# Optimization experiments

Measured on AMD Instinct MI355X. Metric: run time of the kernel, lower is better.

## Reference

```python
import jax, jax.numpy as jnp
import numpy as np

IMG = 4320
FM = 1080            # reduced image size after two stride-2 maxpools
F = 21               # RPN feature map size ((1080-50)//50 + 1)
NUM_ANCHORS = 6
SCALE = (IMG / 4.0) / (IMG / 200.0)   # input_shape/cnn_output_shape = 50.0
CONF = 0.95
K = 5                # bounding_box_limit


def _anchor_boxes():
    sizes = [1.0, 2.0]; ars = [0.5, 1.0, 2.0]
    base = np.array([[0.0, s * -(ar - 1) / 2, s, s * (1 + (ar - 1) / 2)]
                     for s in sizes for ar in ars], np.float32)        # (6,4)
    g = np.arange(F, dtype=np.float32)
    xg = np.broadcast_to(g[:, None], (F, F))
    yg = np.broadcast_to(g[None, :], (F, F))
    pos = np.stack([xg, yg, xg, yg], 0)                                # (4,F,F)
    return jnp.asarray(base[:, :, None, None] + pos[None])             # (6,4,F,F)


def _conv(x, w, b, stride, pad):
    y = jax.lax.conv_general_dilated(x, w, (stride, stride), [(pad, pad), (pad, pad)],
                                     dimension_numbers=('NCHW', 'OIHW', 'NCHW'))
    return y + b[None, :, None, None]


def _maxpool2(x):
    return jax.lax.reduce_window(x, -jnp.inf, jax.lax.max, (1, 1, 2, 2), (1, 1, 2, 2), 'VALID')


def _apply_offsets(a, o):
    # faithful to apply_bounding_box_offsets_to_anchors (note callers swap args)
    return jnp.stack([a[:, 0] + o[:, 0] - o[:, 2] / 2,
                      a[:, 1] - o[:, 3] / 2,
                      a[:, 2] + o[:, 0] + o[:, 2] / 2,
                      a[:, 3] + o[:, 3] / 2], 1)


def _clip(b, h, w):  # torchvision clip_boxes_to_image, size=(h,w)
    return jnp.stack([jnp.clip(b[:, 0], 0, w), jnp.clip(b[:, 1], 0, h),
                      jnp.clip(b[:, 2], 0, w), jnp.clip(b[:, 3], 0, h)], 1)


def _forward(x, conv1_w, conv1_b, conv2_w, conv2_b, conv3_w, conv3_b, conv4_w, conv4_b,
             rpn_conv_w, rpn_conv_b, rpn_bbox_w, rpn_bbox_b, rpn_cls_w, rpn_cls_b,
             fc_w, fc_b, box_w, box_b, cls_w, cls_b):
    # backbone: (conv,conv,maxpool) x2, channels 3->3->2 then 2->2->1
    h = _conv(x, conv1_w, conv1_b, 1, 1)
    h = _maxpool2(_conv(h, conv2_w, conv2_b, 1, 1))
    h = _conv(h, conv3_w, conv3_b, 1, 1)
    reduced = _maxpool2(_conv(h, conv4_w, conv4_b, 1, 1))      # (1,1,1080,1080)

    # ---- RPN ----
    y = _conv(reduced, rpn_conv_w, rpn_conv_b, 50, 0)          # (1,2,21,21)
    offsets = _conv(y, rpn_bbox_w, rpn_bbox_b, 1, 1).reshape(NUM_ANCHORS, 4, F, F)
    obj = jnp.tanh(_conv(y, rpn_cls_w, rpn_cls_b, 1, 1))[0]    # (6,21,21)
    # mask broadcast over coord dim, then masked_select == row-major order of Trues
    mask = jnp.broadcast_to((obj > CONF)[:, None], (NUM_ANCHORS, 4, F, F)).reshape(-1)
    sel = jnp.argsort(jnp.logical_not(mask), stable=True)[: 4 * K]
    anch = _anchor_boxes().reshape(-1)[sel].reshape(K, 4)
    offs = offsets.reshape(-1)[sel].reshape(K, 4)
    # NOTE: source swaps args: anchors<-offsets, offsets<-anchor boxes
    props = _clip(_apply_offsets(offs, anch), F, F) * SCALE    # (5,4)

    # ---- torchvision-style RoIPool (quantized, spatial_scale=1, 2x2) ----
    feat = reduced[0, 0]                                       # (1080,1080)
    x1, y1, x2, y2 = (jnp.round(props[:, i]) for i in range(4))
    bw = jnp.maximum(x2 - x1 + 1, 1.0) / 2.0
    bh = jnp.maximum(y2 - y1 + 1, 1.0) / 2.0
    p = jnp.arange(2, dtype=props.dtype)
    ws = jnp.clip(jnp.floor(p[None] * bw[:, None]) + x1[:, None], 0, FM)   # (5,2)
    we = jnp.clip(jnp.ceil((p[None] + 1) * bw[:, None]) + x1[:, None], 0, FM)
    hs = jnp.clip(jnp.floor(p[None] * bh[:, None]) + y1[:, None], 0, FM)
    he = jnp.clip(jnp.ceil((p[None] + 1) * bh[:, None]) + y1[:, None], 0, FM)
    c = jnp.arange(FM, dtype=props.dtype)
    mw = (c[None, None] >= ws[:, :, None]) & (c[None, None] < we[:, :, None])  # (5,2,FM)
    mh = (c[None, None] >= hs[:, :, None]) & (c[None, None] < he[:, :, None])
    rowmax = jnp.max(jnp.where(mw[:, :, None, :], feat[None, None], -jnp.inf), -1)  # (5,pw,h)
    pooled = jnp.max(jnp.where(mh[:, :, None, :], rowmax[:, None], -jnp.inf), -1)   # (5,ph,pw)
    pooled = jnp.where(jnp.isfinite(pooled), pooled, 0.0).reshape(K, 4)

    # ---- heads ----
    fc = pooled @ fc_w.T + fc_b                                # (5,12)
    box_off = fc @ box_w.T + box_b                             # (5,4)
    # clip to (X.shape[0]=1, X.shape[1]=3) as in source (batch, channels!)
    boxes = _clip(_apply_offsets(props, box_off), x.shape[0], x.shape[1])
    cls = jax.nn.softmax(fc @ cls_w.T + cls_b, axis=1)         # (5,2)
    return boxes[None], cls[None]


def setup_inputs() -> dict:
    key = jax.random.key(0)
    ks = jax.random.split(key, 21)
    n = lambda k, shape, s: jax.random.normal(k, shape, jnp.float32) * s
    return {
        'x': n(ks[0], (1, 3, IMG, IMG), 1.0),
        'conv1_w': n(ks[1], (3, 3, 3, 3), 0.1), 'conv1_b': n(ks[2], (3,), 0.1),
        'conv2_w': n(ks[3], (2, 3, 3, 3), 0.1), 'conv2_b': n(ks[4], (2,), 0.1),
        'conv3_w': n(ks[5], (2, 2, 3, 3), 0.1), 'conv3_b': n(ks[6], (2,), 0.1),
        'conv4_w': n(ks[7], (1, 2, 3, 3), 0.1), 'conv4_b': n(ks[8], (1,), 0.1),
        'rpn_conv_w': n(ks[9], (2, 1, 50, 50), 0.02), 'rpn_conv_b': n(ks[10], (2,), 0.1),
        'rpn_bbox_w': n(ks[11], (24, 2, 3, 3), 0.1), 'rpn_bbox_b': n(ks[12], (24,), 0.1),
        'rpn_cls_w': n(ks[13], (6, 2, 3, 3), 0.001),
        'rpn_cls_b': jnp.full((6,), 2.5, jnp.float32),  # tanh(~2.5)>0.95 -> >=5 proposals guaranteed
        'fc_w': n(ks[15], (12, 4), 0.3), 'fc_b': n(ks[16], (12,), 0.1),
        'box_w': n(ks[17], (4, 12), 0.3), 'box_b': n(ks[18], (4,), 0.1),
        'cls_w': n(ks[19], (2, 12), 0.3), 'cls_b': n(ks[20], (2,), 0.1),
    }


def reference(x, conv1_w, conv1_b, conv2_w, conv2_b, conv3_w, conv3_b, conv4_w, conv4_b,
              rpn_conv_w, rpn_conv_b, rpn_bbox_w, rpn_bbox_b, rpn_cls_w, rpn_cls_b,
              fc_w, fc_b, box_w, box_b, cls_w, cls_b):
    return _forward(x, conv1_w, conv1_b, conv2_w, conv2_b, conv3_w, conv3_b, conv4_w, conv4_b,
                    rpn_conv_w, rpn_conv_b, rpn_bbox_w, rpn_bbox_b, rpn_cls_w, rpn_cls_b,
                    fc_w, fc_b, box_w, box_b, cls_w, cls_b)
```

## Files before the change

kernel.cpp:

```cpp
#include <hip/hip_runtime.h>
#include <math.h>

#define IMG 4320
#define H2D 2160
#define FMD 1080
#define FF 21

typedef unsigned short u16;

__device__ __forceinline__ float bf2f(u16 h) {
  return __uint_as_float(((unsigned)h) << 16);
}
__device__ __forceinline__ u16 f2bf(float f) {
  unsigned u = __float_as_uint(f);
  unsigned r = 0x7FFFu + ((u >> 16) & 1u);
  return (u16)((u + r) >> 16);
}


template<bool REDGE>
__device__ __forceinline__ void conv1_body(
    const int gx, const int gy,
    const float* __restrict__ x, const float* __restrict__ w1,
    const float* __restrict__ b1, u16* __restrict__ c1) {
  const int c0 = gx * 4, r0 = gy * 4;
  const bool okL = gx > 0, okR = gx < 1079;
  float s[6][3][6];
  #pragma unroll
  for (int rr = 0; rr < 6; ++rr) {
    const int row = r0 - 1 + rr;
    const int rowc = REDGE ? (row < 0 ? 0 : (row > IMG - 1 ? IMG - 1 : row)) : row;
    const size_t rbase = (size_t)rowc * IMG + c0;
    #pragma unroll
    for (int ic = 0; ic < 3; ++ic) {
      const float* bp = x + (size_t)ic * IMG * IMG + rbase;
      const float4 q = *(const float4*)bp;
      s[rr][ic][1] = q.x; s[rr][ic][2] = q.y; s[rr][ic][3] = q.z; s[rr][ic][4] = q.w;
      s[rr][ic][0] = bp[okL ? -1 : 0];
      s[rr][ic][5] = bp[okR ? 4 : 0];
    }
  }
  #pragma unroll
  for (int rr = 0; rr < 6; ++rr) {
    const bool rok = REDGE ? ((unsigned)(r0 - 1 + rr) < (unsigned)IMG) : true;
    #pragma unroll
    for (int ic = 0; ic < 3; ++ic) {
      if (REDGE) {
        #pragma unroll
        for (int j = 0; j < 6; ++j) s[rr][ic][j] = rok ? s[rr][ic][j] : 0.f;
      }
      s[rr][ic][0] = okL ? s[rr][ic][0] : 0.f;
      s[rr][ic][5] = okR ? s[rr][ic][5] : 0.f;
    }
  }
  float acc[3][4][4];
  #pragma unroll
  for (int oc = 0; oc < 3; ++oc) {
    const float bb = b1[oc];
    #pragma unroll
    for (int r = 0; r < 4; ++r)
      #pragma unroll
      for (int j = 0; j < 4; ++j) acc[oc][r][j] = bb;
  }
  #pragma unroll
  for (int oc = 0; oc < 3; ++oc)
    #pragma unroll
    for (int ic = 0; ic < 3; ++ic)
      #pragma unroll
      for (int dy = 0; dy < 3; ++dy)
        #pragma unroll
        for (int dx = 0; dx < 3; ++dx) {
          const float w = w1[oc * 27 + ic * 9 + dy * 3 + dx];
          #pragma unroll
          for (int r = 0; r < 4; ++r)
            #pragma unroll
            for (int j = 0; j < 4; ++j)
              acc[oc][r][j] += s[r + dy][ic][j + dx] * w;
        }
  #pragma unroll
  for (int oc = 0; oc < 3; ++oc)
    #pragma unroll
    for (int r = 0; r < 4; ++r) {
      ushort4 h;
      h.x = f2bf(acc[oc][r][0]); h.y = f2bf(acc[oc][r][1]);
      h.z = f2bf(acc[oc][r][2]); h.w = f2bf(acc[oc][r][3]);
      *(ushort4*)(c1 + (size_t)oc * IMG * IMG + (size_t)(r0 + r) * IMG + c0) = h;
    }
}

__global__ __launch_bounds__(256, 2) void k_conv1(
    const float* __restrict__ x, const float* __restrict__ w1,
    const float* __restrict__ b1, u16* __restrict__ c1) {
  const int g = blockIdx.x * 256 + threadIdx.x;
  if (g >= 1080 * 1080) return;
  const int gx = g % 1080, gy = g / 1080;
  const int gy_min = (blockIdx.x * 256) / 1080;
  const int gy_max = (blockIdx.x * 256 + 255) / 1080;
  if (gy_min == 0 || gy_max >= 1079) conv1_body<true>(gx, gy, x, w1, b1, c1);
  else                               conv1_body<false>(gx, gy, x, w1, b1, c1);
}

template<bool REDGE>
__device__ __forceinline__ void conv2_body(
    const int gx, const int gy,
    const u16* __restrict__ c1, const float* __restrict__ w2,
    const float* __restrict__ b2, float* __restrict__ h2) {
  const int c0 = gx * 4, r0 = gy * 4;
  const bool okL = gx > 0, okR = gx < 1079;
  ushort4 mv[6][3];
  u16 lv[6][3], rv[6][3];
  #pragma unroll
  for (int rr = 0; rr < 6; ++rr) {
    const int row = r0 - 1 + rr;
    const int rowc = REDGE ? (row < 0 ? 0 : (row > IMG - 1 ? IMG - 1 : row)) : row;
    const size_t rbase = (size_t)rowc * IMG + c0;
    #pragma unroll
    for (int ic = 0; ic < 3; ++ic) {
      const u16* bp = c1 + (size_t)ic * IMG * IMG + rbase;
      mv[rr][ic] = *(const ushort4*)bp;
      lv[rr][ic] = bp[okL ? -1 : 0];
      rv[rr][ic] = bp[okR ? 4 : 0];
    }
  }
  float s[6][3][6];
  #pragma unroll
  for (int rr = 0; rr < 6; ++rr) {
    const bool rok = REDGE ? ((unsigned)(r0 - 1 + rr) < (unsigned)IMG) : true;
    #pragma unroll
    for (int ic = 0; ic < 3; ++ic) {
      s[rr][ic][0] = (okL && rok) ? bf2f(lv[rr][ic]) : 0.f;
      s[rr][ic][1] = bf2f(mv[rr][ic].x);
      s[rr][ic][2] = bf2f(mv[rr][ic].y);
      s[rr][ic][3] = bf2f(mv[rr][ic].z);
      s[rr][ic][4] = bf2f(mv[rr][ic].w);
      s[rr][ic][5] = (okR && rok) ? bf2f(rv[rr][ic]) : 0.f;
      if (REDGE) {
        #pragma unroll
        for (int j = 1; j < 5; ++j) s[rr][ic][j] = rok ? s[rr][ic][j] : 0.f;
      }
    }
  }
  float pm[2][2][2];
  #pragma unroll
  for (int oc = 0; oc < 2; ++oc)
    #pragma unroll
    for (int a = 0; a < 2; ++a)
      #pragma unroll
      for (int b = 0; b < 2; ++b) pm[oc][a][b] = -INFINITY;
  #pragma unroll
  for (int cr = 0; cr < 4; ++cr) {
    float v[2][4];
    #pragma unroll
    for (int oc = 0; oc < 2; ++oc) {
      const float bb = b2[oc];
      #pragma unroll
      for (int cc = 0; cc < 4; ++cc) v[oc][cc] = bb;
    }
    #pragma unroll
    for (int oc = 0; oc < 2; ++oc)
      #pragma unroll
      for (int ic = 0; ic < 3; ++ic)
        #pragma unroll
        for (int dy = 0; dy < 3; ++dy)
          #pragma unroll
          for (int dx = 0; dx < 3; ++dx) {
            const float w = w2[oc * 27 + ic * 9 + dy * 3 + dx];
            #pragma unroll
            for (int cc = 0; cc < 4; ++cc)
              v[oc][cc] += s[cr + dy][ic][cc + dx] * w;
          }
    #pragma unroll
    for (int oc = 0; oc < 2; ++oc)
      #pragma unroll
      for (int cc = 0; cc < 4; ++cc)
        pm[oc][cr >> 1][cc >> 1] = fmaxf(pm[oc][cr >> 1][cc >> 1], v[oc][cc]);
  }
  #pragma unroll
  for (int oc = 0; oc < 2; ++oc)
    #pragma unroll
    for (int rp = 0; rp < 2; ++rp) {
      float2 o;
      o.x = pm[oc][rp][0];
      o.y = pm[oc][rp][1];
      *(float2*)(h2 + (size_t)oc * H2D * H2D + (size_t)(gy * 2 + rp) * H2D + gx * 2) = o;
    }
}

__global__ __launch_bounds__(256, 2) void k_conv2pool(
    const u16* __restrict__ c1, const float* __restrict__ w2,
    const float* __restrict__ b2, float* __restrict__ h2) {
  const int g = blockIdx.x * 256 + threadIdx.x;
  if (g >= 1080 * 1080) return;
  const int gx = g % 1080, gy = g / 1080;
  const int gy_min = (blockIdx.x * 256) / 1080;
  const int gy_max = (blockIdx.x * 256 + 255) / 1080;
  if (gy_min == 0 || gy_max >= 1079) conv2_body<true>(gx, gy, c1, w2, b2, h2);
  else                               conv2_body<false>(gx, gy, c1, w2, b2, h2);
}

template<bool REDGE>
__device__ __forceinline__ void conv3_body(
    const int gx, const int gy,
    const float* __restrict__ h2, const float* __restrict__ w3,
    const float* __restrict__ b3, float* __restrict__ c3) {
  const int c0 = gx * 4, r0 = gy * 4;
  const bool okL = gx > 0, okR = gx < 539;
  float s[6][2][6];
  #pragma unroll
  for (int rr = 0; rr < 6; ++rr) {
    const int row = r0 - 1 + rr;
    const int rowc = REDGE ? (row < 0 ? 0 : (row > H2D - 1 ? H2D - 1 : row)) : row;
    const size_t rbase = (size_t)rowc * H2D + c0;
    #pragma unroll
    for (int ic = 0; ic < 2; ++ic) {
      const float* bp = h2 + (size_t)ic * H2D * H2D + rbase;
      const float4 q = *(const float4*)bp;
      s[rr][ic][1] = q.x; s[rr][ic][2] = q.y; s[rr][ic][3] = q.z; s[rr][ic][4] = q.w;
      s[rr][ic][0] = bp[okL ? -1 : 0];
      s[rr][ic][5] = bp[okR ? 4 : 0];
    }
  }
  #pragma unroll
  for (int rr = 0; rr < 6; ++rr) {
    const bool rok = REDGE ? ((unsigned)(r0 - 1 + rr) < (unsigned)H2D) : true;
    #pragma unroll
    for (int ic = 0; ic < 2; ++ic) {
      if (REDGE) {
        #pragma unroll
        for (int j = 0; j < 6; ++j) s[rr][ic][j] = rok ? s[rr][ic][j] : 0.f;
      }
      s[rr][ic][0] = okL ? s[rr][ic][0] : 0.f;
      s[rr][ic][5] = okR ? s[rr][ic][5] : 0.f;
    }
  }
  float acc[2][4][4];
  #pragma unroll
  for (int oc = 0; oc < 2; ++oc) {
    const float bb = b3[oc];
    #pragma unroll
    for (int r = 0; r < 4; ++r)
      #pragma unroll
      for (int j = 0; j < 4; ++j) acc[oc][r][j] = bb;
  }
  #pragma unroll
  for (int oc = 0; oc < 2; ++oc)
    #pragma unroll
    for (int ic = 0; ic < 2; ++ic)
      #pragma unroll
      for (int dy = 0; dy < 3; ++dy)
        #pragma unroll
        for (int dx = 0; dx < 3; ++dx) {
          const float w = w3[oc * 18 + ic * 9 + dy * 3 + dx];
          #pragma unroll
          for (int r = 0; r < 4; ++r)
            #pragma unroll
            for (int j = 0; j < 4; ++j)
              acc[oc][r][j] += s[r + dy][ic][j + dx] * w;
        }
  #pragma unroll
  for (int oc = 0; oc < 2; ++oc)
    #pragma unroll
    for (int r = 0; r < 4; ++r) {
      float4 o;
      o.x = acc[oc][r][0]; o.y = acc[oc][r][1];
      o.z = acc[oc][r][2]; o.w = acc[oc][r][3];
      *(float4*)(c3 + (size_t)oc * H2D * H2D + (size_t)(r0 + r) * H2D + c0) = o;
    }
}

__global__ __launch_bounds__(256, 2) void k_conv3(
    const float* __restrict__ h2, const float* __restrict__ w3,
    const float* __restrict__ b3, float* __restrict__ c3) {
  const int g = blockIdx.x * 256 + threadIdx.x;
  if (g >= 540 * 540) return;
  const int gx = g % 540, gy = g / 540;
  const int gy_min = (blockIdx.x * 256) / 540;
  const int gy_max = (blockIdx.x * 256 + 255) / 540;
  if (gy_min == 0 || gy_max >= 539) conv3_body<true>(gx, gy, h2, w3, b3, c3);
  else                              conv3_body<false>(gx, gy, h2, w3, b3, c3);
}

template<bool REDGE>
__device__ __forceinline__ void conv4_body(
    const int gx, const int gy,
    const float* __restrict__ c3, const float* __restrict__ w4,
    const float* __restrict__ b4, float* __restrict__ red) {
  const int c0 = gx * 4, r0 = gy * 4;
  const bool okL = gx > 0, okR = gx < 539;
  float s[6][2][6];
  #pragma unroll
  for (int rr = 0; rr < 6; ++rr) {
    const int row = r0 - 1 + rr;
    const int rowc = REDGE ? (row < 0 ? 0 : (row > H2D - 1 ? H2D - 1 : row)) : row;
    const size_t rbase = (size_t)rowc * H2D + c0;
    #pragma unroll
    for (int ic = 0; ic < 2; ++ic) {
      const float* bp = c3 + (size_t)ic * H2D * H2D + rbase;
      const float4 q = *(const float4*)bp;
      s[rr][ic][1] = q.x; s[rr][ic][2] = q.y; s[rr][ic][3] = q.z; s[rr][ic][4] = q.w;
      s[rr][ic][0] = bp[okL ? -1 : 0];
      s[rr][ic][5] = bp[okR ? 4 : 0];
    }
  }
  #pragma unroll
  for (int rr = 0; rr < 6; ++rr) {
    const bool rok = REDGE ? ((unsigned)(r0 - 1 + rr) < (unsigned)H2D) : true;
    #pragma unroll
    for (int ic = 0; ic < 2; ++ic) {
      if (REDGE) {
        #pragma unroll
        for (int j = 0; j < 6; ++j) s[rr][ic][j] = rok ? s[rr][ic][j] : 0.f;
      }
      s[rr][ic][0] = okL ? s[rr][ic][0] : 0.f;
      s[rr][ic][5] = okR ? s[rr][ic][5] : 0.f;
    }
  }
  float pm[2][2];
  pm[0][0] = pm[0][1] = pm[1][0] = pm[1][1] = -INFINITY;
  const float bb = b4[0];
  #pragma unroll
  for (int cr = 0; cr < 4; ++cr) {
    float v[4];
    #pragma unroll
    for (int cc = 0; cc < 4; ++cc) v[cc] = bb;
    #pragma unroll
    for (int ic = 0; ic < 2; ++ic)
      #pragma unroll
      for (int dy = 0; dy < 3; ++dy)
        #pragma unroll
        for (int dx = 0; dx < 3; ++dx) {
          const float w = w4[ic * 9 + dy * 3 + dx];
          #pragma unroll
          for (int cc = 0; cc < 4; ++cc)
            v[cc] += s[cr + dy][ic][cc + dx] * w;
        }
    #pragma unroll
    for (int cc = 0; cc < 4; ++cc)
      pm[cr >> 1][cc >> 1] = fmaxf(pm[cr >> 1][cc >> 1], v[cc]);
  }
  #pragma unroll
  for (int rp = 0; rp < 2; ++rp) {
    float2 o;
    o.x = pm[rp][0];
    o.y = pm[rp][1];
    *(float2*)(red + (size_t)(gy * 2 + rp) * FMD + gx * 2) = o;
  }
}

__global__ __launch_bounds__(256, 2) void k_conv4pool(
    const float* __restrict__ c3, const float* __restrict__ w4,
    const float* __restrict__ b4, float* __restrict__ red) {
  const int g = blockIdx.x * 256 + threadIdx.x;
  if (g >= 540 * 540) return;
  const int gx = g % 540, gy = g / 540;
  const int gy_min = (blockIdx.x * 256) / 540;
  const int gy_max = (blockIdx.x * 256 + 255) / 540;
  if (gy_min == 0 || gy_max >= 539) conv4_body<true>(gx, gy, c3, w4, b4, red);
  else                              conv4_body<false>(gx, gy, c3, w4, b4, red);
}

__global__ __launch_bounds__(256) void k1_backbone1(
    const float* __restrict__ x,
    const float* __restrict__ w1, const float* __restrict__ b1,
    const float* __restrict__ w2, const float* __restrict__ b2,
    float* __restrict__ h2) {
  __shared__ float xs[3][34][36];
  __shared__ float c1s[3][32][36];
  const int tid = threadIdx.x;
  const int bx = blockIdx.x, by = blockIdx.y;
  const int gy0 = by * 30 - 2, gx0 = bx * 30 - 2;
  float W1[81], B1[3];
  #pragma unroll
  for (int i = 0; i < 81; ++i) W1[i] = w1[i];
  #pragma unroll
  for (int i = 0; i < 3; ++i) B1[i] = b1[i];
  for (int l = tid; l < 3 * 34 * 34; l += 256) {
    int c = l / 1156, rem = l % 1156, r = rem / 34, cc = rem % 34;
    int gy = gy0 + r, gx = gx0 + cc;
    float v = 0.f;
    if ((unsigned)gy < IMG && (unsigned)gx < IMG)
      v = x[(size_t)c * IMG * IMG + (size_t)gy * IMG + gx];
    xs[c][r][cc] = v;
  }
  __syncthreads();
  {
    const int r = tid >> 3;
    const int c4 = (tid & 7) << 2;
    float acc[3][4];
    #pragma unroll
    for (int oc = 0; oc < 3; ++oc)
      #pragma unroll
      for (int j = 0; j < 4; ++j) acc[oc][j] = B1[oc];
    #pragma unroll
    for (int ic = 0; ic < 3; ++ic) {
      float xr[3][8];
      #pragma unroll
      for (int dy = 0; dy < 3; ++dy) {
        const float4 q0 = *(const float4*)&xs[ic][r + dy][c4];
        const float4 q1 = *(const float4*)&xs[ic][r + dy][c4 + 4];
        xr[dy][0] = q0.x; xr[dy][1] = q0.y; xr[dy][2] = q0.z; xr[dy][3] = q0.w;
        xr[dy][4] = q1.x; xr[dy][5] = q1.y; xr[dy][6] = q1.z; xr[dy][7] = q1.w;
      }
      #pragma unroll
      for (int oc = 0; oc < 3; ++oc)
        #pragma unroll
        for (int dy = 0; dy < 3; ++dy)
          #pragma unroll
          for (int dx = 0; dx < 3; ++dx) {
            const float w = W1[oc * 27 + ic * 9 + dy * 3 + dx];
            #pragma unroll
            for (int j = 0; j < 4; ++j) acc[oc][j] += xr[dy][j + dx] * w;
          }
    }
    const int gy = by * 30 - 1 + r;
    const bool rOK = (unsigned)gy < IMG;
    const int gxb = bx * 30 - 1 + c4;
    #pragma unroll
    for (int oc = 0; oc < 3; ++oc) {
      float4 o;
      o.x = (rOK && (unsigned)(gxb + 0) < IMG) ? acc[oc][0] : 0.f;
      o.y = (rOK && (unsigned)(gxb + 1) < IMG) ? acc[oc][1] : 0.f;
      o.z = (rOK && (unsigned)(gxb + 2) < IMG) ? acc[oc][2] : 0.f;
      o.w = (rOK && (unsigned)(gxb + 3) < IMG) ? acc[oc][3] : 0.f;
      *(float4*)&c1s[oc][r][c4] = o;
    }
  }
  __syncthreads();
  float W2[54], B2[2];
  #pragma unroll
  for (int i = 0; i < 54; ++i) W2[i] = w2[i];
  B2[0] = b2[0]; B2[1] = b2[1];
  const int ty = tid >> 4, tx = tid & 15;
  if (ty < 15 && tx < 15) {
    float cr[3][4][4];
    #pragma unroll
    for (int ic = 0; ic < 3; ++ic)
      #pragma unroll
      for (int rr = 0; rr < 4; ++rr) {
        const float2 p0 = *(const float2*)&c1s[ic][2 * ty + rr][2 * tx];
        const float2 p1 = *(const float2*)&c1s[ic][2 * ty + rr][2 * tx + 2];
        cr[ic][rr][0] = p0.x; cr[ic][rr][1] = p0.y;
        cr[ic][rr][2] = p1.x; cr[ic][rr][3] = p1.y;
      }
    float m0 = -INFINITY, m1 = -INFINITY;
    #pragma unroll
    for (int sy = 0; sy < 2; ++sy)
      #pragma unroll
      for (int sx = 0; sx < 2; ++sx) {
        float a0 = B2[0], a1 = B2[1];
        #pragma unroll
        for (int ic = 0; ic < 3; ++ic)
          #pragma unroll
          for (int dy = 0; dy < 3; ++dy)
            #pragma unroll
            for (int dx = 0; dx < 3; ++dx) {
              const float v = cr[ic][sy + dy][sx + dx];
              a0 += v * W2[ic * 9 + dy * 3 + dx];
              a1 += v * W2[27 + ic * 9 + dy * 3 + dx];
            }
        m0 = fmaxf(m0, a0);
        m1 = fmaxf(m1, a1);
      }
    const size_t o = (size_t)(by * 15 + ty) * H2D + (bx * 15 + tx);
    h2[o] = m0;
    h2[(size_t)H2D * H2D + o] = m1;
  }
}

__global__ __launch_bounds__(256) void k2_backbone2(
    const float* __restrict__ h2,
    const float* __restrict__ w3, const float* __restrict__ b3,
    const float* __restrict__ w4, const float* __restrict__ b4,
    float* __restrict__ red) {
  __shared__ float hs[2][34][36];
  __shared__ float c3s[2][32][36];
  const int tid = threadIdx.x;
  const int bx = blockIdx.x, by = blockIdx.y;
  const int gy0 = by * 30 - 2, gx0 = bx * 30 - 2;
  float W3[36], B3[2];
  #pragma unroll
  for (int i = 0; i < 36; ++i) W3[i] = w3[i];
  B3[0] = b3[0]; B3[1] = b3[1];
  for (int l = tid; l < 2 * 34 * 34; l += 256) {
    int c = l / 1156, rem = l % 1156, r = rem / 34, cc = rem % 34;
    int gy = gy0 + r, gx = gx0 + cc;
    float v = 0.f;
    if ((unsigned)gy < H2D && (unsigned)gx < H2D)
      v = h2[(size_t)c * H2D * H2D + (size_t)gy * H2D + gx];
    hs[c][r][cc] = v;
  }
  __syncthreads();
  {
    const int r = tid >> 3;
    const int c4 = (tid & 7) << 2;
    float acc[2][4];
    #pragma unroll
    for (int oc = 0; oc < 2; ++oc)
      #pragma unroll
      for (int j = 0; j < 4; ++j) acc[oc][j] = B3[oc];
    #pragma unroll
    for (int ic = 0; ic < 2; ++ic) {
      float xr[3][8];
      #pragma unroll
      for (int dy = 0; dy < 3; ++dy) {
        const float4 q0 = *(const float4*)&hs[ic][r + dy][c4];
        const float4 q1 = *(const float4*)&hs[ic][r + dy][c4 + 4];
        xr[dy][0] = q0.x; xr[dy][1] = q0.y; xr[dy][2] = q0.z; xr[dy][3] = q0.w;
        xr[dy][4] = q1.x; xr[dy][5] = q1.y; xr[dy][6] = q1.z; xr[dy][7] = q1.w;
      }
      #pragma unroll
      for (int oc = 0; oc < 2; ++oc)
        #pragma unroll
        for (int dy = 0; dy < 3; ++dy)
          #pragma unroll
          for (int dx = 0; dx < 3; ++dx) {
            const float w = W3[oc * 18 + ic * 9 + dy * 3 + dx];
            #pragma unroll
            for (int j = 0; j < 4; ++j) acc[oc][j] += xr[dy][j + dx] * w;
          }
    }
    const int gy = by * 30 - 1 + r;
    const bool rOK = (unsigned)gy < H2D;
    const int gxb = bx * 30 - 1 + c4;
    #pragma unroll
    for (int oc = 0; oc < 2; ++oc) {
      float4 o;
      o.x = (rOK && (unsigned)(gxb + 0) < H2D) ? acc[oc][0] : 0.f;
      o.y = (rOK && (unsigned)(gxb + 1) < H2D) ? acc[oc][1] : 0.f;
      o.z = (rOK && (unsigned)(gxb + 2) < H2D) ? acc[oc][2] : 0.f;
      o.w = (rOK && (unsigned)(gxb + 3) < H2D) ? acc[oc][3] : 0.f;
      *(float4*)&c3s[oc][r][c4] = o;
    }
  }
  __syncthreads();
  float W4[18], B4;
  #pragma unroll
  for (int i = 0; i < 18; ++i) W4[i] = w4[i];
  B4 = b4[0];
  const int ty = tid >> 4, tx = tid & 15;
  if (ty < 15 && tx < 15) {
    float cr[2][4][4];
    #pragma unroll
    for (int ic = 0; ic < 2; ++ic)
      #pragma unroll
      for (int rr = 0; rr < 4; ++rr) {
        const float2 p0 = *(const float2*)&c3s[ic][2 * ty + rr][2 * tx];
        const float2 p1 = *(const float2*)&c3s[ic][2 * ty + rr][2 * tx + 2];
        cr[ic][rr][0] = p0.x; cr[ic][rr][1] = p0.y;
        cr[ic][rr][2] = p1.x; cr[ic][rr][3] = p1.y;
      }
    float m = -INFINITY;
    #pragma unroll
    for (int sy = 0; sy < 2; ++sy)
      #pragma unroll
      for (int sx = 0; sx < 2; ++sx) {
        float a = B4;
        #pragma unroll
        for (int ic = 0; ic < 2; ++ic)
          #pragma unroll
          for (int dy = 0; dy < 3; ++dy)
            #pragma unroll
            for (int dx = 0; dx < 3; ++dx)
              a += cr[ic][sy + dy][sx + dx] * W4[ic * 9 + dy * 3 + dx];
        m = fmaxf(m, a);
      }
    red[(size_t)(by * 15 + ty) * FMD + (bx * 15 + tx)] = m;
  }
}

__global__ __launch_bounds__(256) void k3_rpnconv(
    const float* __restrict__ red,
    const float* __restrict__ w, const float* __restrict__ b,
    float* __restrict__ y) {
  __shared__ float part[256];
  const int cell = blockIdx.x;
  const int i = cell / FF, j = cell % FF;
  const int tid = threadIdx.x;
  float a0 = 0.f, a1 = 0.f;
  for (int t = tid; t < 2500; t += 256) {
    int ay = t / 50, ax = t % 50;
    float v = red[(size_t)(50 * i + ay) * FMD + 50 * j + ax];
    a0 += v * w[t];
    a1 += v * w[2500 + t];
  }
  part[tid] = a0;
  __syncthreads();
  for (int s = 128; s > 0; s >>= 1) {
    if (tid < s) part[tid] += part[tid + s];
    __syncthreads();
  }
  if (tid == 0) y[cell] = part[0] + b[0];
  __syncthreads();
  part[tid] = a1;
  __syncthreads();
  for (int s = 128; s > 0; s >>= 1) {
    if (tid < s) part[tid] += part[tid + s];
    __syncthreads();
  }
  if (tid == 0) y[441 + cell] = part[0] + b[1];
}

__global__ __launch_bounds__(512) void k4_select(
    const float* __restrict__ y,
    const float* __restrict__ bbw, const float* __restrict__ bbb,
    const float* __restrict__ clw, const float* __restrict__ clb,
    float* __restrict__ props_out, int* __restrict__ rects,
    unsigned* __restrict__ pooled_m) {
  __shared__ float ys[2][23][23];
  __shared__ unsigned char flag[6][441];
  __shared__ short pos[6][20];
  __shared__ int cnt[6];
  __shared__ int selT[20];
  __shared__ float offv[20], anchv[20];
  const int tid = threadIdx.x;
  for (int l = tid; l < 2 * 23 * 23; l += 512) ((float*)ys)[l] = 0.f;
  __syncthreads();
  for (int l = tid; l < 2 * 441; l += 512) {
    int c = l / 441, p = l % 441;
    ys[c][p / 21 + 1][p % 21 + 1] = y[l];
  }
  __syncthreads();
  for (int l = tid; l < 6 * 441; l += 512) {
    int a = l / 441, p = l % 441, i = p / 21, j = p % 21;
    float v = clb[a];
    #pragma unroll
    for (int c2 = 0; c2 < 2; c2++)
      #pragma unroll
      for (int dy = 0; dy < 3; dy++)
        #pragma unroll
        for (int dx = 0; dx < 3; dx++)
          v += ys[c2][i + dy][j + dx] * clw[a * 18 + c2 * 9 + dy * 3 + dx];
    flag[a][p] = (tanhf(v) > 0.95f) ? 1 : 0;
  }
  __syncthreads();
  if (tid < 6) {
    int c = 0;
    for (int p = 0; p < 441; p++)
      if (flag[tid][p]) {
        if (c < 20) pos[tid][c] = (short)p;
        c++;
      }
    cnt[tid] = c;
  }
  __syncthreads();
  if (tid == 0) {
    int s = 0;
    for (int g = 0; g < 24 && s < 20; g++) {
      int a = g >> 2;
      int take = cnt[a] < 20 - s ? cnt[a] : 20 - s;
      for (int r = 0; r < take; r++) selT[s++] = g * 441 + (int)pos[a][r];
    }
    if (s < 20) {
      for (int t = 0; t < 10584 && s < 20; t++) {
        int a = t / 1764, p = t % 441;
        if (!flag[a][p]) selT[s++] = t;
      }
    }
  }
  __syncthreads();
  if (tid < 20) {
    int t = selT[tid];
    int ch = t / 441, p = t % 441, i = p / 21, j = p % 21;
    int a = ch >> 2, c = ch & 3;
    float v = bbb[ch];
    #pragma unroll
    for (int c2 = 0; c2 < 2; c2++)
      #pragma unroll
      for (int dy = 0; dy < 3; dy++)
        #pragma unroll
        for (int dx = 0; dx < 3; dx++)
          v += ys[c2][i + dy][j + dx] * bbw[ch * 18 + c2 * 9 + dy * 3 + dx];
    offv[tid] = v;
    float sz = (a < 3) ? 1.f : 2.f;
    int am = a % 3;
    float ar = (am == 0) ? 0.5f : (am == 1 ? 1.f : 2.f);
    float base;
    if (c == 0) base = 0.f;
    else if (c == 1) base = sz * -(ar - 1.f) * 0.5f;
    else if (c == 2) base = sz;
    else base = sz * (1.f + (ar - 1.f) * 0.5f);
    anchv[tid] = base + ((c & 1) ? (float)j : (float)i);
  }
  __syncthreads();
  if (tid < 5) {
    int k = tid;
    float o0 = offv[4 * k], o1 = offv[4 * k + 1], o2 = offv[4 * k + 2], o3 = offv[4 * k + 3];
    float a0 = anchv[4 * k], a2 = anchv[4 * k + 2], a3 = anchv[4 * k + 3];
    float p0 = fminf(fmaxf(o0 + a0 - a2 * 0.5f, 0.f), 21.f) * 50.f;
    float p1 = fminf(fmaxf(o1 - a3 * 0.5f, 0.f), 21.f) * 50.f;
    float p2 = fminf(fmaxf(o2 + a0 + a2 * 0.5f, 0.f), 21.f) * 50.f;
    float p3 = fminf(fmaxf(o3 + a3 * 0.5f, 0.f), 21.f) * 50.f;
    props_out[k * 4 + 0] = p0;
    props_out[k * 4 + 1] = p1;
    props_out[k * 4 + 2] = p2;
    props_out[k * 4 + 3] = p3;
    float x1 = rintf(p0), y1 = rintf(p1), x2 = rintf(p2), y2 = rintf(p3);
    float bwf = fmaxf(x2 - x1 + 1.f, 1.f) * 0.5f;
    float bhf = fmaxf(y2 - y1 + 1.f, 1.f) * 0.5f;
    for (int ph = 0; ph < 2; ph++)
      for (int pw = 0; pw < 2; pw++) {
        int hsv = (int)fminf(fmaxf(floorf((float)ph * bhf) + y1, 0.f), 1080.f);
        int hev = (int)fminf(fmaxf(ceilf((float)(ph + 1) * bhf) + y1, 0.f), 1080.f);
        int wsv = (int)fminf(fmaxf(floorf((float)pw * bwf) + x1, 0.f), 1080.f);
        int wev = (int)fminf(fmaxf(ceilf((float)(pw + 1) * bwf) + x1, 0.f), 1080.f);
        int idx = k * 4 + ph * 2 + pw;
        rects[idx * 4 + 0] = hsv;
        rects[idx * 4 + 1] = hev;
        rects[idx * 4 + 2] = wsv;
        rects[idx * 4 + 3] = wev;
      }
  }
  if (tid >= 32 && tid < 52) pooled_m[tid - 32] = 0x007FFFFFu;
}

__global__ __launch_bounds__(256) void k5_roipool(
    const float* __restrict__ red, const int* __restrict__ rects,
    unsigned* __restrict__ pooled_m) {
  const int cell = blockIdx.x;
  const int hs = rects[cell * 4 + 0], he = rects[cell * 4 + 1];
  const int wss = rects[cell * 4 + 2], wee = rects[cell * 4 + 3];
  const int nr = he - hs;
  if (nr <= 0 || wee <= wss) return;
  const int slice = blockIdx.y, nslice = gridDim.y;
  const int r0 = hs + (int)((long)nr * slice / nslice);
  const int r1 = hs + (int)((long)nr * (slice + 1) / nslice);
  float m = -INFINITY;
  for (int r = r0; r < r1; r++)
    for (int c = wss + (int)threadIdx.x; c < wee; c += 256)
      m = fmaxf(m, red[(size_t)r * FMD + c]);
  __shared__ float part[256];
  part[threadIdx.x] = m;
  __syncthreads();
  for (int s = 128; s > 0; s >>= 1) {
    if ((int)threadIdx.x < s) part[threadIdx.x] = fmaxf(part[threadIdx.x], part[threadIdx.x + s]);
    __syncthreads();
  }
  if (threadIdx.x == 0 && part[0] > -INFINITY) {
    unsigned u = __float_as_uint(part[0]);
    u = (u & 0x80000000u) ? ~u : (u | 0x80000000u);
    atomicMax(&pooled_m[cell], u);
  }
}

__global__ void k6_heads(
    const unsigned* __restrict__ pooled_m, const float* __restrict__ props,
    const float* __restrict__ fcw, const float* __restrict__ fcb,
    const float* __restrict__ bxw, const float* __restrict__ bxb,
    const float* __restrict__ clw, const float* __restrict__ clb,
    float* __restrict__ out) {
  if (threadIdx.x != 0 || blockIdx.x != 0) return;
  float pooled[5][4];
  for (int i = 0; i < 20; i++) {
    unsigned u = pooled_m[i];
    float f = (u & 0x80000000u) ? __uint_as_float(u ^ 0x80000000u) : __uint_as_float(~u);
    if (!isfinite(f)) f = 0.f;
    pooled[i / 4][i % 4] = f;
  }
  for (int k = 0; k < 5; k++) {
    float fc[12];
    for (int m = 0; m < 12; m++) {
      float v = fcb[m];
      for (int n = 0; n < 4; n++) v += pooled[k][n] * fcw[m * 4 + n];
      fc[m] = v;
    }
    float bo[4];
    for (int c = 0; c < 4; c++) {
      float v = bxb[c];
      for (int m = 0; m < 12; m++) v += fc[m] * bxw[c * 12 + m];
      bo[c] = v;
    }
    float p0 = props[k * 4], p1 = props[k * 4 + 1], p2 = props[k * 4 + 2], p3 = props[k * 4 + 3];
    out[k * 4 + 0] = fminf(fmaxf(p0 + bo[0] - bo[2] * 0.5f, 0.f), 3.f);
    out[k * 4 + 1] = fminf(fmaxf(p1 - bo[3] * 0.5f, 0.f), 1.f);
    out[k * 4 + 2] = fminf(fmaxf(p2 + bo[0] + bo[2] * 0.5f, 0.f), 3.f);
    out[k * 4 + 3] = fminf(fmaxf(p3 + bo[3] * 0.5f, 0.f), 1.f);
    float l0 = clb[0], l1 = clb[1];
    for (int m = 0; m < 12; m++) {
      l0 += fc[m] * clw[m];
      l1 += fc[m] * clw[12 + m];
    }
    float mx = fmaxf(l0, l1);
    float e0 = expf(l0 - mx), e1 = expf(l1 - mx);
    out[20 + k * 2 + 0] = e0 / (e0 + e1);
    out[20 + k * 2 + 1] = e1 / (e0 + e1);
  }
}

extern "C" void kernel_launch(void* const* d_in, const int* in_sizes, int n_in,
                              void* d_out, int out_size, void* d_ws, size_t ws_size,
                              hipStream_t stream) {
  const float* x   = (const float*)d_in[0];
  const float* w1  = (const float*)d_in[1];
  const float* b1  = (const float*)d_in[2];
  const float* w2  = (const float*)d_in[3];
  const float* b2  = (const float*)d_in[4];
  const float* w3  = (const float*)d_in[5];
  const float* b3  = (const float*)d_in[6];
  const float* w4  = (const float*)d_in[7];
  const float* b4  = (const float*)d_in[8];
  const float* rw  = (const float*)d_in[9];
  const float* rb  = (const float*)d_in[10];
  const float* bbw = (const float*)d_in[11];
  const float* bbb = (const float*)d_in[12];
  const float* clw = (const float*)d_in[13];
  const float* clb = (const float*)d_in[14];
  const float* fcw = (const float*)d_in[15];
  const float* fcb = (const float*)d_in[16];
  const float* bxw = (const float*)d_in[17];
  const float* bxb = (const float*)d_in[18];
  const float* c2w = (const float*)d_in[19];
  const float* c2b = (const float*)d_in[20];

  char* wsb = (char*)d_ws;

  if (ws_size >= 160000000ull) {
    u16*   c1u = (u16*)wsb;
    float* h2  = (float*)(wsb + 111974400);
    float* c3  = (float*)wsb;
    float* red = (float*)(wsb + 149299200);
    float* yv  = (float*)(wsb + 153964800);
    float* props = yv + 882;
    int*   rects = (int*)(props + 20);
    unsigned* pooled_m = (unsigned*)(rects + 80);

    k_conv1    <<<4557, 256, 0, stream>>>(x, w1, b1, c1u);
    k_conv2pool<<<4557, 256, 0, stream>>>(c1u, w2, b2, h2);
    k_conv3    <<<1140, 256, 0, stream>>>(h2, w3, b3, c3);
    k_conv4pool<<<1140, 256, 0, stream>>>(c3, w4, b4, red);
    k3_rpnconv<<<441, 256, 0, stream>>>(red, rw, rb, yv);
    k4_select<<<1, 512, 0, stream>>>(yv, bbw, bbb, clw, clb, props, rects, pooled_m);
    k5_roipool<<<dim3(20, 16), 256, 0, stream>>>(red, rects, pooled_m);
    k6_heads<<<1, 64, 0, stream>>>(pooled_m, props, fcw, fcb, bxw, bxb, c2w, c2b,
                                   (float*)d_out);
  } else {
    float* ws = (float*)d_ws;
    float* h2 = ws;
    float* red = ws + 9331200;
    float* yv = ws + 10497600;
    float* props = ws + 10498482;
    int* rects = (int*)(ws + 10498502);
    unsigned* pooled_m = (unsigned*)(ws + 10498582);

    k1_backbone1<<<dim3(144, 144), 256, 0, stream>>>(x, w1, b1, w2, b2, h2);
    k2_backbone2<<<dim3(72, 72), 256, 0, stream>>>(h2, w3, b3, w4, b4, red);
    k3_rpnconv<<<441, 256, 0, stream>>>(red, rw, rb, yv);
    k4_select<<<1, 512, 0, stream>>>(yv, bbw, bbb, clw, clb, props, rects, pooled_m);
    k5_roipool<<<dim3(20, 16), 256, 0, stream>>>(red, rects, pooled_m);
    k6_heads<<<1, 64, 0, stream>>>(pooled_m, props, fcw, fcb, bxw, bxb, c2w, c2b,
                                   (float*)d_out);
  }
}
```

Baseline: 224.6 us.

## Widen conv2 tiles to 8 columns and fuse conv3+conv4 via shared-memory kernel

conv2+pool threads now each compute an 8-column strip instead of 4, which halves the thread count and amortizes halo loads. The separate conv3 and conv4pool kernels on the large-workspace path are replaced by the existing tiled k2_backbone2 kernel. It keeps the conv3 intermediate in shared memory, so the full-resolution c3 tensor no longer makes a round trip through global memory. The costs are higher register pressure in conv2 and some redundant halo compute in the fused tile kernel.

```diff
diff --git a/kernel.cpp b/kernel.cpp
--- a/kernel.cpp
+++ b/kernel.cpp
@@ -16,7 +16,6 @@
   unsigned r = 0x7FFFu + ((u >> 16) & 1u);
   return (u16)((u + r) >> 16);
 }
-
 
 template<bool REDGE>
 __device__ __forceinline__ void conv1_body(
@@ -105,10 +104,10 @@
     const int gx, const int gy,
     const u16* __restrict__ c1, const float* __restrict__ w2,
     const float* __restrict__ b2, float* __restrict__ h2) {
-  const int c0 = gx * 4, r0 = gy * 4;
-  const bool okL = gx > 0, okR = gx < 1079;
-  ushort4 mv[6][3];
-  u16 lv[6][3], rv[6][3];
+  const int c0 = gx * 8, r0 = gy * 4;
+  const bool okL = gx > 0, okR = gx < 539;
+  ushort4 q0v[6][3], q1v[6][3];
+  u16 hl[6][3], hr[6][3];
   #pragma unroll
   for (int rr = 0; rr < 6; ++rr) {
     const int row = r0 - 1 + rr;
@@ -117,44 +116,49 @@
     #pragma unroll
     for (int ic = 0; ic < 3; ++ic) {
       const u16* bp = c1 + (size_t)ic * IMG * IMG + rbase;
-      mv[rr][ic] = *(const ushort4*)bp;
-      lv[rr][ic] = bp[okL ? -1 : 0];
-      rv[rr][ic] = bp[okR ? 4 : 0];
-    }
-  }
-  float s[6][3][6];
+      q0v[rr][ic] = *(const ushort4*)bp;
+      q1v[rr][ic] = *(const ushort4*)(bp + 4);
+      hl[rr][ic] = bp[okL ? -1 : 0];
+      hr[rr][ic] = bp[okR ? 8 : 0];
+    }
+  }
+  float s[6][3][10];
   #pragma unroll
   for (int rr = 0; rr < 6; ++rr) {
     const bool rok = REDGE ? ((unsigned)(r0 - 1 + rr) < (unsigned)IMG) : true;
     #pragma unroll
     for (int ic = 0; ic < 3; ++ic) {
-      s[rr][ic][0] = (okL && rok) ? bf2f(lv[rr][ic]) : 0.f;
-      s[rr][ic][1] = bf2f(mv[rr][ic].x);
-      s[rr][ic][2] = bf2f(mv[rr][ic].y);
-      s[rr][ic][3] = bf2f(mv[rr][ic].z);
-      s[rr][ic][4] = bf2f(mv[rr][ic].w);
-      s[rr][ic][5] = (okR && rok) ? bf2f(rv[rr][ic]) : 0.f;
+      s[rr][ic][0] = (okL && rok) ? bf2f(hl[rr][ic]) : 0.f;
+      s[rr][ic][1] = bf2f(q0v[rr][ic].x);
+      s[rr][ic][2] = bf2f(q0v[rr][ic].y);
+      s[rr][ic][3] = bf2f(q0v[rr][ic].z);
+      s[rr][ic][4] = bf2f(q0v[rr][ic].w);
+      s[rr][ic][5] = bf2f(q1v[rr][ic].x);
+      s[rr][ic][6] = bf2f(q1v[rr][ic].y);
+      s[rr][ic][7] = bf2f(q1v[rr][ic].z);
+      s[rr][ic][8] = bf2f(q1v[rr][ic].w);
+      s[rr][ic][9] = (okR && rok) ? bf2f(hr[rr][ic]) : 0.f;
       if (REDGE) {
         #pragma unroll
-        for (int j = 1; j < 5; ++j) s[rr][ic][j] = rok ? s[rr][ic][j] : 0.f;
-      }
-    }
-  }
-  float pm[2][2][2];
+        for (int j = 1; j < 9; ++j) s[rr][ic][j] = rok ? s[rr][ic][j] : 0.f;
+      }
+    }
+  }
+  float pm[2][2][4];
   #pragma unroll
   for (int oc = 0; oc < 2; ++oc)
     #pragma unroll
     for (int a = 0; a < 2; ++a)
       #pragma unroll
-      for (int b = 0; b < 2; ++b) pm[oc][a][b] = -INFINITY;
+      for (int b = 0; b < 4; ++b) pm[oc][a][b] = -INFINITY;
   #pragma unroll
   for (int cr = 0; cr < 4; ++cr) {
-    float v[2][4];
+    float v[2][8];
     #pragma unroll
     for (int oc = 0; oc < 2; ++oc) {
       const float bb = b2[oc];
       #pragma unroll
-      for (int cc = 0; cc < 4; ++cc) v[oc][cc] = bb;
+      for (int cc = 0; cc < 8; ++cc) v[oc][cc] = bb;
     }
     #pragma unroll
     for (int oc = 0; oc < 2; ++oc)
@@ -166,23 +170,23 @@
           for (int dx = 0; dx < 3; ++dx) {
             const float w = w2[oc * 27 + ic * 9 + dy * 3 + dx];
             #pragma unroll
-            for (int cc = 0; cc < 4; ++cc)
+            for (int cc = 0; cc < 8; ++cc)
               v[oc][cc] += s[cr + dy][ic][cc + dx] * w;
           }
     #pragma unroll
     for (int oc = 0; oc < 2; ++oc)
       #pragma unroll
-      for (int cc = 0; cc < 4; ++cc)
+      for (int cc = 0; cc < 8; ++cc)
         pm[oc][cr >> 1][cc >> 1] = fmaxf(pm[oc][cr >> 1][cc >> 1], v[oc][cc]);
   }
   #pragma unroll
   for (int oc = 0; oc < 2; ++oc)
     #pragma unroll
     for (int rp = 0; rp < 2; ++rp) {
-      float2 o;
-      o.x = pm[oc][rp][0];
-      o.y = pm[oc][rp][1];
-      *(float2*)(h2 + (size_t)oc * H2D * H2D + (size_t)(gy * 2 + rp) * H2D + gx * 2) = o;
+      float4 o;
+      o.x = pm[oc][rp][0]; o.y = pm[oc][rp][1];
+      o.z = pm[oc][rp][2]; o.w = pm[oc][rp][3];
+      *(float4*)(h2 + (size_t)oc * H2D * H2D + (size_t)(gy * 2 + rp) * H2D + gx * 4) = o;
     }
 }
 
@@ -190,173 +194,113 @@
     const u16* __restrict__ c1, const float* __restrict__ w2,
     const float* __restrict__ b2, float* __restrict__ h2) {
   const int g = blockIdx.x * 256 + threadIdx.x;
-  if (g >= 1080 * 1080) return;
-  const int gx = g % 1080, gy = g / 1080;
-  const int gy_min = (blockIdx.x * 256) / 1080;
-  const int gy_max = (blockIdx.x * 256 + 255) / 1080;
-  if (gy_min == 0 || gy_max >= 1079) conv2_body<true>(gx, gy, c1, w2, b2, h2);
-  else                               conv2_body<false>(gx, gy, c1, w2, b2, h2);
-}
-
-template<bool REDGE>
-__device__ __forceinline__ void conv3_body(
-    const int gx, const int gy,
-    const float* __restrict__ h2, const float* __restrict__ w3,
-    const float* __restrict__ b3, float* __restrict__ c3) {
-  const int c0 = gx * 4, r0 = gy * 4;
-  const bool okL = gx > 0, okR = gx < 539;
-  float s[6][2][6];
-  #pragma unroll
-  for (int rr = 0; rr < 6; ++rr) {
-    const int row = r0 - 1 + rr;
-    const int rowc = REDGE ? (row < 0 ? 0 : (row > H2D - 1 ? H2D - 1 : row)) : row;
-    const size_t rbase = (size_t)rowc * H2D + c0;
-    #pragma unroll
-    for (int ic = 0; ic < 2; ++ic) {
-      const float* bp = h2 + (size_t)ic * H2D * H2D + rbase;
-      const float4 q = *(const float4*)bp;
-      s[rr][ic][1] = q.x; s[rr][ic][2] = q.y; s[rr][ic][3] = q.z; s[rr][ic][4] = q.w;
-      s[rr][ic][0] = bp[okL ? -1 : 0];
-      s[rr][ic][5] = bp[okR ? 4 : 0];
-    }
-  }
-  #pragma unroll
-  for (int rr = 0; rr < 6; ++rr) {
-    const bool rok = REDGE ? ((unsigned)(r0 - 1 + rr) < (unsigned)H2D) : true;
-    #pragma unroll
-    for (int ic = 0; ic < 2; ++ic) {
-      if (REDGE) {
-        #pragma unroll
-        for (int j = 0; j < 6; ++j) s[rr][ic][j] = rok ? s[rr][ic][j] : 0.f;
-      }
-      s[rr][ic][0] = okL ? s[rr][ic][0] : 0.f;
-      s[rr][ic][5] = okR ? s[rr][ic][5] : 0.f;
-    }
-  }
-  float acc[2][4][4];
-  #pragma unroll
-  for (int oc = 0; oc < 2; ++oc) {
-    const float bb = b3[oc];
-    #pragma unroll
-    for (int r = 0; r < 4; ++r)
-      #pragma unroll
-      for (int j = 0; j < 4; ++j) acc[oc][r][j] = bb;
-  }
-  #pragma unroll
-  for (int oc = 0; oc < 2; ++oc)
-    #pragma unroll
-    for (int ic = 0; ic < 2; ++ic)
-      #pragma unroll
-      for (int dy = 0; dy < 3; ++dy)
-        #pragma unroll
-        for (int dx = 0; dx < 3; ++dx) {
-          const float w = w3[oc * 18 + ic * 9 + dy * 3 + dx];
-          #pragma unroll
-          for (int r = 0; r < 4; ++r)
-            #pragma unroll
-            for (int j = 0; j < 4; ++j)
-              acc[oc][r][j] += s[r + dy][ic][j + dx] * w;
-        }
-  #pragma unroll
-  for (int oc = 0; oc < 2; ++oc)
-    #pragma unroll
-    for (int r = 0; r < 4; ++r) {
-      float4 o;
-      o.x = acc[oc][r][0]; o.y = acc[oc][r][1];
-      o.z = acc[oc][r][2]; o.w = acc[oc][r][3];
-      *(float4*)(c3 + (size_t)oc * H2D * H2D + (size_t)(r0 + r) * H2D + c0) = o;
-    }
-}
-
-__global__ __launch_bounds__(256, 2) void k_conv3(
-    const float* __restrict__ h2, const float* __restrict__ w3,
-    const float* __restrict__ b3, float* __restrict__ c3) {
-  const int g = blockIdx.x * 256 + threadIdx.x;
-  if (g >= 540 * 540) return;
+  if (g >= 540 * 1080) return;
   const int gx = g % 540, gy = g / 540;
   const int gy_min = (blockIdx.x * 256) / 540;
   const int gy_max = (blockIdx.x * 256 + 255) / 540;
-  if (gy_min == 0 || gy_max >= 539) conv3_body<true>(gx, gy, h2, w3, b3, c3);
-  else                              conv3_body<false>(gx, gy, h2, w3, b3, c3);
-}
-
-template<bool REDGE>
-__device__ __forceinline__ void conv4_body(
-    const int gx, const int gy,
-    const float* __restrict__ c3, const float* __restrict__ w4,
-    const float* __restrict__ b4, float* __restrict__ red) {
-  const int c0 = gx * 4, r0 = gy * 4;
-  const bool okL = gx > 0, okR = gx < 539;
-  float s[6][2][6];
-  #pragma unroll
-  for (int rr = 0; rr < 6; ++rr) {
-    const int row = r0 - 1 + rr;
-    const int rowc = REDGE ? (row < 0 ? 0 : (row > H2D - 1 ? H2D - 1 : row)) : row;
-    const size_t rbase = (size_t)rowc * H2D + c0;
+  if (gy_min == 0 || gy_max >= 1079) conv2_body<true>(gx, gy, c1, w2, b2, h2);
+  else                               conv2_body<false>(gx, gy, c1, w2, b2, h2);
+}
+
+__global__ __launch_bounds__(256) void k2_backbone2(
+    const float* __restrict__ h2,
+    const float* __restrict__ w3, const float* __restrict__ b3,
+    const float* __restrict__ w4, const float* __restrict__ b4,
+    float* __restrict__ red) {
+  __shared__ float hs[2][34][36];
+  __shared__ float c3s[2][32][36];
+  const int tid = threadIdx.x;
+  const int bx = blockIdx.x, by = blockIdx.y;
+  const int gy0 = by * 30 - 2, gx0 = bx * 30 - 2;
+  float W3[36], B3[2];
+  #pragma unroll
+  for (int i = 0; i < 36; ++i) W3[i] = w3[i];
+  B3[0] = b3[0]; B3[1] = b3[1];
+  for (int l = tid; l < 2 * 34 * 34; l += 256) {
+    int c = l / 1156, rem = l % 1156, r = rem / 34, cc = rem % 34;
+    int gy = gy0 + r, gx = gx0 + cc;
+    float v = 0.f;
+    if ((unsigned)gy < H2D && (unsigned)gx < H2D)
+      v = h2[(size_t)c * H2D * H2D + (size_t)gy * H2D + gx];
+    hs[c][r][cc] = v;
+  }
+  __syncthreads();
+  {
+    const int r = tid >> 3;
+    const int c4 = (tid & 7) << 2;
+    float acc[2][4];
+    #pragma unroll
+    for (int oc = 0; oc < 2; ++oc)
+      #pragma unroll
+      for (int j = 0; j < 4; ++j) acc[oc][j] = B3[oc];
     #pragma unroll
     for (int ic = 0; ic < 2; ++ic) {
-      const float* bp = c3 + (size_t)ic * H2D * H2D + rbase;
-      const float4 q = *(const float4*)bp;
-      s[rr][ic][1] = q.x; s[rr][ic][2] = q.y; s[rr][ic][3] = q.z; s[rr][ic][4] = q.w;
-      s[rr][ic][0] = bp[okL ? -1 : 0];
-      s[rr][ic][5] = bp[okR ? 4 : 0];
-    }
-  }
-  #pragma unroll
-  for (int rr = 0; rr < 6; ++rr) {
-    const bool rok = REDGE ? ((unsigned)(r0 - 1 + rr) < (unsigned)H2D) : true;
-    #pragma unroll
-    for (int ic = 0; ic < 2; ++ic) {
-      if (REDGE) {
-        #pragma unroll
-        for (int j = 0; j < 6; ++j) s[rr][ic][j] = rok ? s[rr][ic][j] : 0.f;
-      }
-      s[rr][ic][0] = okL ? s[rr][ic][0] : 0.f;
-      s[rr][ic][5] = okR ? s[rr][ic][5] : 0.f;
-    }
-  }
-  float pm[2][2];
-  pm[0][0] = pm[0][1] = pm[1][0] = pm[1][1] = -INFINITY;
-  const float bb = b4[0];
-  #pragma unroll
-  for (int cr = 0; cr < 4; ++cr) {
-    float v[4];
-    #pragma unroll
-    for (int cc = 0; cc < 4; ++cc) v[cc] = bb;
+      float xr[3][8];
+      #pragma unroll
+      for (int dy = 0; dy < 3; ++dy) {
+        const float4 q0 = *(const float4*)&hs[ic][r + dy][c4];
+        const float4 q1 = *(const float4*)&hs[ic][r + dy][c4 + 4];
+        xr[dy][0] = q0.x; xr[dy][1] = q0.y; xr[dy][2] = q0.z; xr[dy][3] = q0.w;
+        xr[dy][4] = q1.x; xr[dy][5] = q1.y; xr[dy][6] = q1.z; xr[dy][7] = q1.w;
+      }
+      #pragma unroll
+      for (int oc = 0; oc < 2; ++oc)
+        #pragma unroll
+        for (int dy = 0; dy < 3; ++dy)
+          #pragma unroll
+          for (int dx = 0; dx < 3; ++dx) {
+            const float w = W3[oc * 18 + ic * 9 + dy * 3 + dx];
+            #pragma unroll
+            for (int j = 0; j < 4; ++j) acc[oc][j] += xr[dy][j + dx] * w;
+          }
+    }
+    const int gy = by * 30 - 1 + r;
+    const bool rOK = (unsigned)gy < H2D;
+    const int gxb = bx * 30 - 1 + c4;
+    #pragma unroll
+    for (int oc = 0; oc < 2; ++oc) {
+      float4 o;
+      o.x = (rOK && (unsigned)(gxb + 0) < H2D) ? acc[oc][0] : 0.f;
+      o.y = (rOK && (unsigned)(gxb + 1) < H2D) ? acc[oc][1] : 0.f;
+      o.z = (rOK && (unsigned)(gxb + 2) < H2D) ? acc[oc][2] : 0.f;
+      o.w = (rOK && (unsigned)(gxb + 3) < H2D) ? acc[oc][3] : 0.f;
+      *(float4*)&c3s[oc][r][c4] = o;
+    }
+  }
+  __syncthreads();
+  float W4[18], B4;
+  #pragma unroll
+  for (int i = 0; i < 18; ++i) W4[i] = w4[i];
+  B4 = b4[0];
+  const int ty = tid >> 4, tx = tid & 15;
+  if (ty < 15 && tx < 15) {
+    float cr[2][4][4];
     #pragma unroll
     for (int ic = 0; ic < 2; ++ic)
       #pragma unroll
-      for (int dy = 0; dy < 3; ++dy)
-        #pragma unroll
-        for (int dx = 0; dx < 3; ++dx) {
-          const float w = w4[ic * 9 + dy * 3 + dx];
+      for (int rr = 0; rr < 4; ++rr) {
+        const float2 p0 = *(const float2*)&c3s[ic][2 * ty + rr][2 * tx];
+        const float2 p1 = *(const float2*)&c3s[ic][2 * ty + rr][2 * tx + 2];
+        cr[ic][rr][0] = p0.x; cr[ic][rr][1] = p0.y;
+        cr[ic][rr][2] = p1.x; cr[ic][rr][3] = p1.y;
+      }
+    float m = -INFINITY;
+    #pragma unroll
+    for (int sy = 0; sy < 2; ++sy)
+      #pragma unroll
+      for (int sx = 0; sx < 2; ++sx) {
+        float a = B4;
+        #pragma unroll
+        for (int ic = 0; ic < 2; ++ic)
           #pragma unroll
-          for (int cc = 0; cc < 4; ++cc)
-            v[cc] += s[cr + dy][ic][cc + dx] * w;
-        }
-    #pragma unroll
-    for (int cc = 0; cc < 4; ++cc)
-      pm[cr >> 1][cc >> 1] = fmaxf(pm[cr >> 1][cc >> 1], v[cc]);
-  }
-  #pragma unroll
-  for (int rp = 0; rp < 2; ++rp) {
-    float2 o;
-    o.x = pm[rp][0];
-    o.y = pm[rp][1];
-    *(float2*)(red + (size_t)(gy * 2 + rp) * FMD + gx * 2) = o;
-  }
-}
-
-__global__ __launch_bounds__(256, 2) void k_conv4pool(
-    const float* __restrict__ c3, const float* __restrict__ w4,
-    const float* __restrict__ b4, float* __restrict__ red) {
-  const int g = blockIdx.x * 256 + threadIdx.x;
-  if (g >= 540 * 540) return;
-  const int gx = g % 540, gy = g / 540;
-  const int gy_min = (blockIdx.x * 256) / 540;
-  const int gy_max = (blockIdx.x * 256 + 255) / 540;
-  if (gy_min == 0 || gy_max >= 539) conv4_body<true>(gx, gy, c3, w4, b4, red);
-  else                              conv4_body<false>(gx, gy, c3, w4, b4, red);
+          for (int dy = 0; dy < 3; ++dy)
+            #pragma unroll
+            for (int dx = 0; dx < 3; ++dx)
+              a += cr[ic][sy + dy][sx + dx] * W4[ic * 9 + dy * 3 + dx];
+        m = fmaxf(m, a);
+      }
+    red[(size_t)(by * 15 + ty) * FMD + (bx * 15 + tx)] = m;
+  }
 }
 
 __global__ __launch_bounds__(256) void k1_backbone1(
@@ -464,107 +408,6 @@
     const size_t o = (size_t)(by * 15 + ty) * H2D + (bx * 15 + tx);
     h2[o] = m0;
     h2[(size_t)H2D * H2D + o] = m1;
-  }
-}
-
-__global__ __launch_bounds__(256) void k2_backbone2(
-    const float* __restrict__ h2,
-    const float* __restrict__ w3, const float* __restrict__ b3,
-    const float* __restrict__ w4, const float* __restrict__ b4,
-    float* __restrict__ red) {
-  __shared__ float hs[2][34][36];
-  __shared__ float c3s[2][32][36];
-  const int tid = threadIdx.x;
-  const int bx = blockIdx.x, by = blockIdx.y;
-  const int gy0 = by * 30 - 2, gx0 = bx * 30 - 2;
-  float W3[36], B3[2];
-  #pragma unroll
-  for (int i = 0; i < 36; ++i) W3[i] = w3[i];
-  B3[0] = b3[0]; B3[1] = b3[1];
-  for (int l = tid; l < 2 * 34 * 34; l += 256) {
-    int c = l / 1156, rem = l % 1156, r = rem / 34, cc = rem % 34;
-    int gy = gy0 + r, gx = gx0 + cc;
-    float v = 0.f;
-    if ((unsigned)gy < H2D && (unsigned)gx < H2D)
-      v = h2[(size_t)c * H2D * H2D + (size_t)gy * H2D + gx];
-    hs[c][r][cc] = v;
-  }
-  __syncthreads();
-  {
-    const int r = tid >> 3;
-    const int c4 = (tid & 7) << 2;
-    float acc[2][4];
-    #pragma unroll
-    for (int oc = 0; oc < 2; ++oc)
-      #pragma unroll
-      for (int j = 0; j < 4; ++j) acc[oc][j] = B3[oc];
-    #pragma unroll
-    for (int ic = 0; ic < 2; ++ic) {
-      float xr[3][8];
-      #pragma unroll
-      for (int dy = 0; dy < 3; ++dy) {
-        const float4 q0 = *(const float4*)&hs[ic][r + dy][c4];
-        const float4 q1 = *(const float4*)&hs[ic][r + dy][c4 + 4];
-        xr[dy][0] = q0.x; xr[dy][1] = q0.y; xr[dy][2] = q0.z; xr[dy][3] = q0.w;
-        xr[dy][4] = q1.x; xr[dy][5] = q1.y; xr[dy][6] = q1.z; xr[dy][7] = q1.w;
-      }
-      #pragma unroll
-      for (int oc = 0; oc < 2; ++oc)
-        #pragma unroll
-        for (int dy = 0; dy < 3; ++dy)
-          #pragma unroll
-          for (int dx = 0; dx < 3; ++dx) {
-            const float w = W3[oc * 18 + ic * 9 + dy * 3 + dx];
-            #pragma unroll
-            for (int j = 0; j < 4; ++j) acc[oc][j] += xr[dy][j + dx] * w;
-          }
-    }
-    const int gy = by * 30 - 1 + r;
-    const bool rOK = (unsigned)gy < H2D;
-    const int gxb = bx * 30 - 1 + c4;
-    #pragma unroll
-    for (int oc = 0; oc < 2; ++oc) {
-      float4 o;
-      o.x = (rOK && (unsigned)(gxb + 0) < H2D) ? acc[oc][0] : 0.f;
-      o.y = (rOK && (unsigned)(gxb + 1) < H2D) ? acc[oc][1] : 0.f;
-      o.z = (rOK && (unsigned)(gxb + 2) < H2D) ? acc[oc][2] : 0.f;
-      o.w = (rOK && (unsigned)(gxb + 3) < H2D) ? acc[oc][3] : 0.f;
-      *(float4*)&c3s[oc][r][c4] = o;
-    }
-  }
-  __syncthreads();
-  float W4[18], B4;
-  #pragma unroll
-  for (int i = 0; i < 18; ++i) W4[i] = w4[i];
-  B4 = b4[0];
-  const int ty = tid >> 4, tx = tid & 15;
-  if (ty < 15 && tx < 15) {
-    float cr[2][4][4];
-    #pragma unroll
-    for (int ic = 0; ic < 2; ++ic)
-      #pragma unroll
-      for (int rr = 0; rr < 4; ++rr) {
-        const float2 p0 = *(const float2*)&c3s[ic][2 * ty + rr][2 * tx];
-        const float2 p1 = *(const float2*)&c3s[ic][2 * ty + rr][2 * tx + 2];
-        cr[ic][rr][0] = p0.x; cr[ic][rr][1] = p0.y;
-        cr[ic][rr][2] = p1.x; cr[ic][rr][3] = p1.y;
-      }
-    float m = -INFINITY;
-    #pragma unroll
-    for (int sy = 0; sy < 2; ++sy)
-      #pragma unroll
-      for (int sx = 0; sx < 2; ++sx) {
-        float a = B4;
-        #pragma unroll
-        for (int ic = 0; ic < 2; ++ic)
-          #pragma unroll
-          for (int dy = 0; dy < 3; ++dy)
-            #pragma unroll
-            for (int dx = 0; dx < 3; ++dx)
-              a += cr[ic][sy + dy][sx + dx] * W4[ic * 9 + dy * 3 + dx];
-        m = fmaxf(m, a);
-      }
-    red[(size_t)(by * 15 + ty) * FMD + (bx * 15 + tx)] = m;
   }
 }
 
@@ -816,7 +659,6 @@
   if (ws_size >= 160000000ull) {
     u16*   c1u = (u16*)wsb;
     float* h2  = (float*)(wsb + 111974400);
-    float* c3  = (float*)wsb;
     float* red = (float*)(wsb + 149299200);
     float* yv  = (float*)(wsb + 153964800);
     float* props = yv + 882;
@@ -824,9 +666,8 @@
     unsigned* pooled_m = (unsigned*)(rects + 80);
 
     k_conv1    <<<4557, 256, 0, stream>>>(x, w1, b1, c1u);
-    k_conv2pool<<<4557, 256, 0, stream>>>(c1u, w2, b2, h2);
-    k_conv3    <<<1140, 256, 0, stream>>>(h2, w3, b3, c3);
-    k_conv4pool<<<1140, 256, 0, stream>>>(c3, w4, b4, red);
+    k_conv2pool<<<2279, 256, 0, stream>>>(c1u, w2, b2, h2);
+    k2_backbone2<<<dim3(72, 72), 256, 0, stream>>>(h2, w3, b3, w4, b4, red);
     k3_rpnconv<<<441, 256, 0, stream>>>(red, rw, rb, yv);
     k4_select<<<1, 512, 0, stream>>>(yv, bbw, bbb, clw, clb, props, rects, pooled_m);
     k5_roipool<<<dim3(20, 16), 256, 0, stream>>>(red, rects, pooled_m);
```

Result: no change. 222.7 us (-0.8%).
